# Kernel optimization log

Hardware: AMD Instinct MI355X
Metric: run time of the kernel (lower is better)

Reference implementation:

```python
import jax, jax.numpy as jnp
import numpy as np

# Static per-expert capacities (tokens are laid out contiguously per expert)
CAPS = [1024, 512, 1024, 256, 1024, 512, 128, 1024, 512, 1024, 256, 512, 1024, 128, 64, 512]
TOTAL = sum(CAPS)  # 9536
E, H, I = 16, 1024, 4096
OFFSETS = np.concatenate([[0], np.cumsum(CAPS)])


def setup_inputs() -> dict:
    key = jax.random.key(0)
    ks = jax.random.split(key, 5)
    x = jax.random.normal(ks[0], (TOTAL, H), dtype=jnp.float32)
    W1 = jax.random.normal(ks[1], (E, I, H), dtype=jnp.float32) * 0.02
    b1 = jax.random.normal(ks[2], (E, I), dtype=jnp.float32) * 0.02
    W2 = jax.random.normal(ks[3], (E, H, I), dtype=jnp.float32) * 0.02
    b2 = jax.random.normal(ks[4], (E, H), dtype=jnp.float32) * 0.02
    return {"x": x, "W1": W1, "b1": b1, "W2": W2, "b2": b2}


def reference(x, W1, b1, W2, b2):
    # Grouped GEMM FFN: expert e processes rows [OFFSETS[e]:OFFSETS[e+1]]
    # out = gelu(x_e @ W1[e].T + b1[e]) @ W2[e].T + b2[e]
    outs = []
    for e in range(E):  # fixed, static loop over experts (capacities are static)
        xs = x[OFFSETS[e]:OFFSETS[e + 1]]                      # [cap_e, H]
        h = jax.nn.gelu(xs @ W1[e].T + b1[e], approximate=False)  # [cap_e, I]
        outs.append(h @ W2[e].T + b2[e])                       # [cap_e, H]
    return jnp.concatenate(outs, axis=0)                       # [TOTAL, H]
```

## Files before the change

### kernel.cpp

```cpp
#include <hip/hip_runtime.h>
#include <math.h>

typedef __attribute__((ext_vector_type(8))) short short8;
typedef __attribute__((ext_vector_type(4))) float f32x4;
typedef __attribute__((ext_vector_type(2))) unsigned int u32x2;
typedef __attribute__((ext_vector_type(4))) unsigned int u32x4;

#define E_NUM 16
constexpr int CAPS[E_NUM] = {1024,512,1024,256,1024,512,128,1024,512,1024,256,512,1024,128,64,512};
constexpr int OFFS[E_NUM] = {0,1024,1536,2560,2816,3840,4352,4480,5504,6016,7040,7296,7808,8832,8960,9024};
constexpr int cdiv_(int a, int b){ return (a + b - 1) / b; }
constexpr int ilog2_(int v){ int l = 0; while ((1 << l) < v) ++l; return l; }

__device__ __forceinline__ unsigned int cvt_pk_bf16(float a, float b){
  unsigned int r;
  asm("v_cvt_pk_bf16_f32 %0, %1, %2" : "=v"(r) : "v"(a), "v"(b));
  return r;
}

typedef __attribute__((address_space(1))) const unsigned char gas_u8;
typedef __attribute__((address_space(3))) unsigned char las_u8;
__device__ __forceinline__ void gl_lds16(const void* g, void* l){
  __builtin_amdgcn_global_load_lds((gas_u8*)g, (las_u8*)l, 16, 0, 0);
}

__global__ __launch_bounds__(256) void cvt_bf16_kernel(const float* __restrict__ x,
                                                       unsigned short* __restrict__ xb, int n8)
{
  int i = blockIdx.x * blockDim.x + threadIdx.x;
  const int stride = gridDim.x * blockDim.x;
  for (; i < n8; i += stride) {
    f32x4 a = *reinterpret_cast<const f32x4*>(x + (size_t)i * 8);
    f32x4 b = *reinterpret_cast<const f32x4*>(x + (size_t)i * 8 + 4);
    u32x2 lo, hi;
    lo[0] = cvt_pk_bf16(a[0], a[1]); lo[1] = cvt_pk_bf16(a[2], a[3]);
    hi[0] = cvt_pk_bf16(b[0], b[1]); hi[1] = cvt_pk_bf16(b[2], b[3]);
    *reinterpret_cast<u32x2*>(xb + (size_t)i * 8)     = lo;
    *reinterpret_cast<u32x2*>(xb + (size_t)i * 8 + 4) = hi;
  }
}

template<int NDIM, int KDIM, int LOG_GN, int NWG>
__device__ __forceinline__ void g1_body(int braw, const unsigned short* __restrict__ Ah,
                                        const float* __restrict__ W,
                                        const float* __restrict__ bias,
                                        unsigned short* __restrict__ Oh, char* smem)
{
  constexpr int A_BYTES = 256 * 64;
  constexpr int B_BYTES = 256 * 128;
  constexpr int BUF  = A_BYTES + B_BYTES;
  constexpr int GN   = 1 << LOG_GN;
  constexpr int NTT  = KDIM / 32;
  static_assert(NWG % 8 == 0);
  static_assert(NTT >= 3);

  const int tid = threadIdx.x;
  const int tt = (braw & 7) * (NWG / 8) + (braw >> 3);

  int m0 = 0, n0 = 0, Me = 0, tok0 = 0;
  size_t wbase = 0, bbase = 0;
  {
    int acc0 = 0;
    #pragma unroll
    for (int i = 0; i < E_NUM; ++i) {
      const int mt  = cdiv_(CAPS[i], 256);
      const int lmt = ilog2_(mt);
      const int nb  = mt * (NDIM / 256);
      if (tt >= acc0 && tt < acc0 + nb) {
        const int loc = tt - acc0;
        const int g   = loc >> (lmt + LOG_GN);
        const int rem = loc & ((mt << LOG_GN) - 1);
        m0   = (rem >> LOG_GN) * 256;
        n0   = ((g << LOG_GN) | (rem & (GN - 1))) * 256;
        Me   = CAPS[i];
        tok0 = OFFS[i];
        wbase = (size_t)i * NDIM * KDIM;
        bbase = (size_t)i * NDIM;
      }
      acc0 += nb;
    }
  }
  const float* Wb = W + wbase;

  const int lane = tid & 63;
  const int wv   = tid >> 6;

  auto stageA = [&](int buf, int kt) {
    const unsigned short* Ag = Ah + (size_t)(tok0 + m0) * KDIM + kt * 32;
    char* dst0 = smem + buf * BUF;
    #pragma unroll
    for (int j = 0; j < 2; ++j) {
      const int rbase = j * 128 + wv * 16;
      const int r     = rbase + (lane >> 2);
      const int blk   = (lane & 3) ^ (r & 3);
      gl_lds16((const void*)(Ag + (size_t)r * KDIM + blk * 8), (void*)(dst0 + rbase * 64));
    }
  };
  auto stageB = [&](int buf, int kt) {
    const float* Bg = Wb + (size_t)n0 * KDIM + kt * 32;
    char* dst0 = smem + buf * BUF + A_BYTES;
    #pragma unroll
    for (int j = 0; j < 4; ++j) {
      const int rbase = j * 64 + wv * 8;
      const int r     = rbase + (lane >> 3);
      const int blk   = (lane & 7) ^ (r & 7);
      gl_lds16((const void*)(Bg + (size_t)r * KDIM + blk * 4), (void*)(dst0 + rbase * 128));
    }
  };

  const int wm   = (wv >> 2) * 128;
  const int wn   = (wv & 3) * 64;
  const int lrow = lane & 15;
  const int pa0  = (((lane >> 4) ^ (lane & 3)) << 4);
  const int pb0  = ((((lane >> 4) << 1) ^ (lane & 7)) << 4);

  f32x4 acc_[8][4];
  #pragma unroll
  for (int i = 0; i < 8; ++i)
    #pragma unroll
    for (int j = 0; j < 4; ++j)
      acc_[i][j] = (f32x4){0.f, 0.f, 0.f, 0.f};

  auto compute = [&](int cur) {
    const char* ab  = smem + cur * BUF;
    const char* bbp = smem + cur * BUF + A_BYTES;
    short8 bfr[4];
    #pragma unroll
    for (int f = 0; f < 4; ++f) {
      const char* rowp = bbp + (size_t)(wn + f * 16 + lrow) * 128;
      f32x4 lo = *reinterpret_cast<const f32x4*>(rowp + pb0);
      f32x4 hi = *reinterpret_cast<const f32x4*>(rowp + (pb0 ^ 16));
      u32x4 pk;
      pk[0] = cvt_pk_bf16(lo[0], lo[1]); pk[1] = cvt_pk_bf16(lo[2], lo[3]);
      pk[2] = cvt_pk_bf16(hi[0], hi[1]); pk[3] = cvt_pk_bf16(hi[2], hi[3]);
      bfr[f] = __builtin_bit_cast(short8, pk);
    }
    #pragma unroll
    for (int i = 0; i < 8; ++i) {
      short8 afr = *reinterpret_cast<const short8*>(ab + (wm + i * 16 + lrow) * 64 + pa0);
      #pragma unroll
      for (int j = 0; j < 4; ++j)
        acc_[i][j] = __builtin_amdgcn_mfma_f32_16x16x32_bf16(afr, bfr[j], acc_[i][j], 0, 0, 0);
    }
  };

  stageA(0, 0); stageB(0, 0);
  stageA(1, 1); stageB(1, 1);
  int cur = 0, nx2 = 2;
  for (int kt = 0; kt < NTT; ++kt) {
    if (kt + 1 < NTT) asm volatile("s_waitcnt vmcnt(6)\n\ts_barrier" ::: "memory");
    else              asm volatile("s_waitcnt vmcnt(0)\n\ts_barrier" ::: "memory");
    __builtin_amdgcn_sched_barrier(0);
    if (kt + 2 < NTT) { stageA(nx2, kt + 2); stageB(nx2, kt + 2); }
    compute(cur);
    cur = (cur == 2) ? 0 : cur + 1;
    nx2 = (nx2 == 2) ? 0 : nx2 + 1;
  }

  float bv[4];
  #pragma unroll
  for (int f = 0; f < 4; ++f)
    bv[f] = bias[bbase + n0 + wn + f * 16 + lrow];

  __syncthreads();
  unsigned short* hout = (unsigned short*)smem;
  #pragma unroll
  for (int i = 0; i < 8; ++i) {
    const int rbase = wm + i * 16 + (lane >> 4) * 4;
    #pragma unroll
    for (int j = 0; j < 4; ++j) {
      #pragma unroll
      for (int jj = 0; jj < 4; ++jj) {
        float xv = acc_[i][j][jj] + bv[j];
        float y2 = xv * (1.5957691216057308f + 0.07135481627f * xv * xv);
        float g  = xv * __builtin_amdgcn_rcpf(1.0f + __expf(-y2));
        hout[(rbase + jj) * 256 + wn + j * 16 + lrow] = (unsigned short)(cvt_pk_bf16(g, g) & 0xFFFFu);
      }
    }
  }
  __syncthreads();
  #pragma unroll
  for (int s = 0; s < 16; ++s) {
    const int row = s * 16 + (tid >> 5);
    const int c   = (tid & 31) * 8;
    if (m0 + row < Me) {
      *reinterpret_cast<short8*>(Oh + (size_t)(tok0 + m0 + row) * NDIM + n0 + c)
        = *reinterpret_cast<const short8*>(hout + row * 256 + c);
    }
  }
}

constexpr int G1_NWG  = 624;
constexpr int CVT_NWG = 640;

__global__ __launch_bounds__(512, 2)
void g1cvt(const unsigned short* __restrict__ xb, const float* __restrict__ W1,
           const float* __restrict__ b1, unsigned short* __restrict__ h,
           const float* __restrict__ W2, unsigned short* __restrict__ w2b)
{
  __shared__ __align__(16) char smem[3 * (256 * 64 + 256 * 128)];
  if ((int)blockIdx.x < G1_NWG) {
    g1_body<4096, 1024, 2, G1_NWG>(blockIdx.x, xb, W1, b1, h, smem);
  } else {
    constexpr int N8 = 16 * 1024 * 4096 / 8;
    int i = ((int)blockIdx.x - G1_NWG) * 512 + (int)threadIdx.x;
    const int stride = CVT_NWG * 512;
    for (; i < N8; i += stride) {
      f32x4 a = *reinterpret_cast<const f32x4*>(W2 + (size_t)i * 8);
      f32x4 b = *reinterpret_cast<const f32x4*>(W2 + (size_t)i * 8 + 4);
      u32x2 lo, hi;
      lo[0] = cvt_pk_bf16(a[0], a[1]); lo[1] = cvt_pk_bf16(a[2], a[3]);
      hi[0] = cvt_pk_bf16(b[0], b[1]); hi[1] = cvt_pk_bf16(b[2], b[3]);
      *reinterpret_cast<u32x2*>(w2b + (size_t)i * 8)     = lo;
      *reinterpret_cast<u32x2*>(w2b + (size_t)i * 8 + 4) = hi;
    }
  }
}

template<int NDIM, int KDIM, int NWG, int KS>
__global__ __launch_bounds__(512, 1)
void g2_gemm256b(const unsigned short* __restrict__ Ah, const unsigned short* __restrict__ Wh,
                 const float* __restrict__ bias, float* __restrict__ Of)
{
  constexpr int T_BYTES = 256 * 64;
  constexpr int BUF  = 2 * T_BYTES;
  constexpr int NT   = KDIM / (KS * 32);
  constexpr int NWG1 = NWG / KS;
  static_assert(NWG % 8 == 0);
  static_assert(NT >= 3);

  __shared__ __align__(16) char smem[3 * BUF];

  const int tid  = threadIdx.x;
  const int braw = blockIdx.x;
  const int t = (braw & 7) * (NWG / 8) + (braw >> 3);

  const int kc    = t / NWG1;
  const int tt    = t % NWG1;
  const int kbase = kc * (KDIM / KS);

  int m0 = 0, n0 = 0, Me = 0, tok0 = 0;
  size_t wbase = 0, bbase = 0;
  {
    int acc0 = 0;
    #pragma unroll
    for (int i = 0; i < E_NUM; ++i) {
      const int mt = cdiv_(CAPS[i], 256);
      const int nb = mt * (NDIM / 256);
      if (tt >= acc0 && tt < acc0 + nb) {
        const int loc = tt - acc0;
        m0   = (loc & (mt - 1)) * 256;
        n0   = (loc >> ilog2_(mt)) * 256;
        Me   = CAPS[i];
        tok0 = OFFS[i];
        wbase = (size_t)i * NDIM * KDIM;
        bbase = (size_t)i * NDIM;
      }
      acc0 += nb;
    }
  }

  const int lane = tid & 63;
  const int wv   = tid >> 6;

  const unsigned short* Abase = Ah + (size_t)(tok0 + m0) * KDIM + kbase;
  const unsigned short* Bbase = Wh + wbase + (size_t)n0 * KDIM + kbase;

  auto stage_tile = [&](const unsigned short* base, char* dst0, int kt) {
    const unsigned short* Tg = base + kt * 32;
    #pragma unroll
    for (int j = 0; j < 2; ++j) {
      const int rbase = wv * 32 + j * 16;
      const int r     = rbase + (lane >> 2);
      const int blk   = (lane & 3) ^ (r & 3);
      gl_lds16((const void*)(Tg + (size_t)r * KDIM + blk * 8), (void*)(dst0 + rbase * 64));
    }
  };
  auto stage = [&](int buf, int kt) {
    stage_tile(Abase, smem + buf * BUF, kt);
    stage_tile(Bbase, smem + buf * BUF + T_BYTES, kt);
  };

  const int wm   = (wv >> 2) * 128;
  const int wn   = (wv & 3) * 64;
  const int lrow = lane & 15;
  const int pa0  = (((lane >> 4) ^ (lane & 3)) << 4);

  f32x4 acc_[8][4];
  #pragma unroll
  for (int i = 0; i < 8; ++i)
    #pragma unroll
    for (int j = 0; j < 4; ++j)
      acc_[i][j] = (f32x4){0.f, 0.f, 0.f, 0.f};

  auto compute = [&](int cur) {
    const char* ab = smem + cur * BUF;
    const char* bb = smem + cur * BUF + T_BYTES;
    short8 bfr[4];
    #pragma unroll
    for (int f = 0; f < 4; ++f)
      bfr[f] = *reinterpret_cast<const short8*>(bb + (wn + f * 16 + lrow) * 64 + pa0);
    #pragma unroll
    for (int i = 0; i < 8; ++i) {
      short8 afr = *reinterpret_cast<const short8*>(ab + (wm + i * 16 + lrow) * 64 + pa0);
      #pragma unroll
      for (int j = 0; j < 4; ++j)
        acc_[i][j] = __builtin_amdgcn_mfma_f32_16x16x32_bf16(afr, bfr[j], acc_[i][j], 0, 0, 0);
    }
  };

  stage(0, 0);
  stage(1, 1);
  int cur = 0, nx2 = 2;
  for (int kt = 0; kt < NT; ++kt) {
    if (kt + 1 < NT) asm volatile("s_waitcnt vmcnt(4)\n\ts_barrier" ::: "memory");
    else             asm volatile("s_waitcnt vmcnt(0)\n\ts_barrier" ::: "memory");
    __builtin_amdgcn_sched_barrier(0);
    if (kt + 2 < NT) stage(nx2, kt + 2);
    compute(cur);
    cur = (cur == 2) ? 0 : cur + 1;
    nx2 = (nx2 == 2) ? 0 : nx2 + 1;
  }

  float bv[4];
  #pragma unroll
  for (int f = 0; f < 4; ++f)
    bv[f] = bias[bbase + n0 + wn + f * 16 + lrow];

  constexpr float BS = 1.0f / (float)KS;
  #pragma unroll
  for (int i = 0; i < 8; ++i) {
    const int rbase = wm + i * 16 + (lane >> 4) * 4;
    #pragma unroll
    for (int jj = 0; jj < 4; ++jj) {
      int grow = m0 + rbase + jj;
      if (grow < Me) {
        #pragma unroll
        for (int j = 0; j < 4; ++j) {
          float v = acc_[i][j][jj] + bv[j] * BS;
          unsafeAtomicAdd(Of + (size_t)(tok0 + grow) * NDIM + n0 + wn + j * 16 + lrow, v);
        }
      }
    }
  }
}

extern "C" void kernel_launch(void* const* d_in, const int* in_sizes, int n_in,
                              void* d_out, int out_size, void* d_ws, size_t ws_size,
                              hipStream_t stream)
{
  const float* x  = (const float*)d_in[0];
  const float* W1 = (const float*)d_in[1];
  const float* b1 = (const float*)d_in[2];
  const float* W2 = (const float*)d_in[3];
  const float* b2 = (const float*)d_in[4];
  float* out = (float*)d_out;

  constexpr size_t H_BYTES   = (size_t)9536 * 4096 * 2;
  constexpr size_t XB_BYTES  = (size_t)9536 * 1024 * 2;
  unsigned short* h   = (unsigned short*)d_ws;
  unsigned short* xb  = (unsigned short*)((char*)d_ws + H_BYTES);
  unsigned short* w2b = (unsigned short*)((char*)d_ws + H_BYTES + XB_BYTES);

  hipMemsetAsync(d_out, 0, (size_t)out_size * sizeof(float), stream);

  cvt_bf16_kernel<<<2048, 256, 0, stream>>>(x, xb, 9536 * 1024 / 8);

  g1cvt<<<G1_NWG + CVT_NWG, 512, 0, stream>>>(xb, W1, b1, h, W2, w2b);

  g2_gemm256b<1024, 4096, 624, 4><<<624, 512, 0, stream>>>(h, w2b, b2, out);
}
```

Before: 417.2 us.

## Split W2 conversion from GEMM1 and retile GEMM2 to 128x128 with split-K 2

Undoes the fused GEMM1 plus W2-conversion kernel: GEMM1 becomes its own kernel and W2 is converted by a separate launch of the generic bf16 conversion kernel. GEMM2 moves from 256x256 tiles with a 3-stage pipeline and split-K 4 to 128x128 tiles, 256 threads, double buffering, split-K 2 and 1200 workgroups, so that more blocks can fit per CU. The aim is better occupancy and fewer atomic adds in GEMM2. In exchange it loses the overlap between the W2 conversion and GEMM1, re-reads operands more often because the tiles are smaller, and uses a simpler synchronisation scheme with a full barrier every K step.

New measurement: 424.8 us. Within noise of the previous version (+1.8%).

```diff
diff --git a/kernel.cpp b/kernel.cpp
--- a/kernel.cpp
+++ b/kernel.cpp
@@ -41,10 +41,9 @@
 }
 
 template<int NDIM, int KDIM, int LOG_GN, int NWG>
-__device__ __forceinline__ void g1_body(int braw, const unsigned short* __restrict__ Ah,
-                                        const float* __restrict__ W,
-                                        const float* __restrict__ bias,
-                                        unsigned short* __restrict__ Oh, char* smem)
+__global__ __launch_bounds__(512, 2)
+void g1_gemm256(const unsigned short* __restrict__ Ah, const float* __restrict__ W,
+                const float* __restrict__ bias, unsigned short* __restrict__ Oh)
 {
   constexpr int A_BYTES = 256 * 64;
   constexpr int B_BYTES = 256 * 128;
@@ -54,7 +53,10 @@
   static_assert(NWG % 8 == 0);
   static_assert(NTT >= 3);
 
-  const int tid = threadIdx.x;
+  __shared__ __align__(16) char smem[3 * BUF];
+
+  const int tid  = threadIdx.x;
+  const int braw = blockIdx.x;
   const int tt = (braw & 7) * (NWG / 8) + (braw >> 3);
 
   int m0 = 0, n0 = 0, Me = 0, tok0 = 0;
@@ -190,46 +192,19 @@
   }
 }
 
-constexpr int G1_NWG  = 624;
-constexpr int CVT_NWG = 640;
-
-__global__ __launch_bounds__(512, 2)
-void g1cvt(const unsigned short* __restrict__ xb, const float* __restrict__ W1,
-           const float* __restrict__ b1, unsigned short* __restrict__ h,
-           const float* __restrict__ W2, unsigned short* __restrict__ w2b)
-{
-  __shared__ __align__(16) char smem[3 * (256 * 64 + 256 * 128)];
-  if ((int)blockIdx.x < G1_NWG) {
-    g1_body<4096, 1024, 2, G1_NWG>(blockIdx.x, xb, W1, b1, h, smem);
-  } else {
-    constexpr int N8 = 16 * 1024 * 4096 / 8;
-    int i = ((int)blockIdx.x - G1_NWG) * 512 + (int)threadIdx.x;
-    const int stride = CVT_NWG * 512;
-    for (; i < N8; i += stride) {
-      f32x4 a = *reinterpret_cast<const f32x4*>(W2 + (size_t)i * 8);
-      f32x4 b = *reinterpret_cast<const f32x4*>(W2 + (size_t)i * 8 + 4);
-      u32x2 lo, hi;
-      lo[0] = cvt_pk_bf16(a[0], a[1]); lo[1] = cvt_pk_bf16(a[2], a[3]);
-      hi[0] = cvt_pk_bf16(b[0], b[1]); hi[1] = cvt_pk_bf16(b[2], b[3]);
-      *reinterpret_cast<u32x2*>(w2b + (size_t)i * 8)     = lo;
-      *reinterpret_cast<u32x2*>(w2b + (size_t)i * 8 + 4) = hi;
-    }
-  }
-}
-
 template<int NDIM, int KDIM, int NWG, int KS>
-__global__ __launch_bounds__(512, 1)
-void g2_gemm256b(const unsigned short* __restrict__ Ah, const unsigned short* __restrict__ Wh,
+__global__ __launch_bounds__(256, 5)
+void g2_gemm128b(const unsigned short* __restrict__ Ah, const unsigned short* __restrict__ Wh,
                  const float* __restrict__ bias, float* __restrict__ Of)
 {
-  constexpr int T_BYTES = 256 * 64;
+  constexpr int T_BYTES = 128 * 64;
   constexpr int BUF  = 2 * T_BYTES;
   constexpr int NT   = KDIM / (KS * 32);
   constexpr int NWG1 = NWG / KS;
   static_assert(NWG % 8 == 0);
-  static_assert(NT >= 3);
-
-  __shared__ __align__(16) char smem[3 * BUF];
+  static_assert(NT >= 2);
+
+  __shared__ __align__(16) char smem[2 * BUF];
 
   const int tid  = threadIdx.x;
   const int braw = blockIdx.x;
@@ -245,12 +220,12 @@
     int acc0 = 0;
     #pragma unroll
     for (int i = 0; i < E_NUM; ++i) {
-      const int mt = cdiv_(CAPS[i], 256);
-      const int nb = mt * (NDIM / 256);
+      const int mt = cdiv_(CAPS[i], 128);
+      const int nb = mt * (NDIM / 128);
       if (tt >= acc0 && tt < acc0 + nb) {
         const int loc = tt - acc0;
-        m0   = (loc & (mt - 1)) * 256;
-        n0   = (loc >> ilog2_(mt)) * 256;
+        m0   = (loc & (mt - 1)) * 128;
+        n0   = (loc >> ilog2_(mt)) * 128;
         Me   = CAPS[i];
         tok0 = OFFS[i];
         wbase = (size_t)i * NDIM * KDIM;
@@ -262,6 +237,10 @@
 
   const int lane = tid & 63;
   const int wv   = tid >> 6;
+  const int wm   = (wv >> 1) * 64;
+  const int wn   = (wv & 1) * 64;
+  const int lrow = lane & 15;
+  const int pa0  = (((lane >> 4) ^ (lane & 3)) << 4);
 
   const unsigned short* Abase = Ah + (size_t)(tok0 + m0) * KDIM + kbase;
   const unsigned short* Bbase = Wh + wbase + (size_t)n0 * KDIM + kbase;
@@ -281,14 +260,9 @@
     stage_tile(Bbase, smem + buf * BUF + T_BYTES, kt);
   };
 
-  const int wm   = (wv >> 2) * 128;
-  const int wn   = (wv & 3) * 64;
-  const int lrow = lane & 15;
-  const int pa0  = (((lane >> 4) ^ (lane & 3)) << 4);
-
-  f32x4 acc_[8][4];
-  #pragma unroll
-  for (int i = 0; i < 8; ++i)
+  f32x4 acc_[4][4];
+  #pragma unroll
+  for (int i = 0; i < 4; ++i)
     #pragma unroll
     for (int j = 0; j < 4; ++j)
       acc_[i][j] = (f32x4){0.f, 0.f, 0.f, 0.f};
@@ -296,30 +270,27 @@
   auto compute = [&](int cur) {
     const char* ab = smem + cur * BUF;
     const char* bb = smem + cur * BUF + T_BYTES;
-    short8 bfr[4];
+    short8 afr[4], bfr[4];
+    #pragma unroll
+    for (int f = 0; f < 4; ++f)
+      afr[f] = *reinterpret_cast<const short8*>(ab + (wm + f * 16 + lrow) * 64 + pa0);
     #pragma unroll
     for (int f = 0; f < 4; ++f)
       bfr[f] = *reinterpret_cast<const short8*>(bb + (wn + f * 16 + lrow) * 64 + pa0);
     #pragma unroll
-    for (int i = 0; i < 8; ++i) {
-      short8 afr = *reinterpret_cast<const short8*>(ab + (wm + i * 16 + lrow) * 64 + pa0);
+    for (int i = 0; i < 4; ++i)
       #pragma unroll
       for (int j = 0; j < 4; ++j)
-        acc_[i][j] = __builtin_amdgcn_mfma_f32_16x16x32_bf16(afr, bfr[j], acc_[i][j], 0, 0, 0);
-    }
+        acc_[i][j] = __builtin_amdgcn_mfma_f32_16x16x32_bf16(afr[i], bfr[j], acc_[i][j], 0, 0, 0);
   };
 
   stage(0, 0);
-  stage(1, 1);
-  int cur = 0, nx2 = 2;
+  __syncthreads();
   for (int kt = 0; kt < NT; ++kt) {
-    if (kt + 1 < NT) asm volatile("s_waitcnt vmcnt(4)\n\ts_barrier" ::: "memory");
-    else             asm volatile("s_waitcnt vmcnt(0)\n\ts_barrier" ::: "memory");
-    __builtin_amdgcn_sched_barrier(0);
-    if (kt + 2 < NT) stage(nx2, kt + 2);
+    const int cur = kt & 1;
+    if (kt + 1 < NT) stage(cur ^ 1, kt + 1);
     compute(cur);
-    cur = (cur == 2) ? 0 : cur + 1;
-    nx2 = (nx2 == 2) ? 0 : nx2 + 1;
+    __syncthreads();
   }
 
   float bv[4];
@@ -329,7 +300,7 @@
 
   constexpr float BS = 1.0f / (float)KS;
   #pragma unroll
-  for (int i = 0; i < 8; ++i) {
+  for (int i = 0; i < 4; ++i) {
     const int rbase = wm + i * 16 + (lane >> 4) * 4;
     #pragma unroll
     for (int jj = 0; jj < 4; ++jj) {
@@ -338,7 +309,9 @@
         #pragma unroll
         for (int j = 0; j < 4; ++j) {
           float v = acc_[i][j][jj] + bv[j] * BS;
-          unsafeAtomicAdd(Of + (size_t)(tok0 + grow) * NDIM + n0 + wn + j * 16 + lrow, v);
+          float* p = Of + (size_t)(tok0 + grow) * NDIM + n0 + wn + j * 16 + lrow;
+          if constexpr (KS > 1) unsafeAtomicAdd(p, v);
+          else                  *p = v;
         }
       }
     }
@@ -366,7 +339,9 @@
 
   cvt_bf16_kernel<<<2048, 256, 0, stream>>>(x, xb, 9536 * 1024 / 8);
 
-  g1cvt<<<G1_NWG + CVT_NWG, 512, 0, stream>>>(xb, W1, b1, h, W2, w2b);
-
-  g2_gemm256b<1024, 4096, 624, 4><<<624, 512, 0, stream>>>(h, w2b, b2, out);
-}
+  g1_gemm256<4096, 1024, 2, 624><<<624, 512, 0, stream>>>(xb, W1, b1, h);
+
+  cvt_bf16_kernel<<<2048, 256, 0, stream>>>(W2, w2b, 16 * 1024 * 4096 / 8);
+
+  g2_gemm128b<1024, 4096, 1200, 2><<<1200, 256, 0, stream>>>(h, w2b, b2, out);
+}
```
